# Optimization experiments

Hardware: AMD Instinct MI355X
Metric: run time of the kernel (lower is better)

## Reference

```python
import jax, jax.numpy as jnp
import numpy as np

N_NODES = 50000
N_GRAPHS = 64
BN_EPS = 1e-5
DIMS = [128, 256, 128, 64]


def setup_inputs() -> dict:
    key = jax.random.key(0)
    ks = jax.random.split(key, 32)
    inp = {}
    inp['x'] = jax.random.normal(ks[0], (N_NODES, DIMS[0]), dtype=jnp.float32)
    inp['edge_index'] = jax.random.randint(ks[1], (2, 800000), 0, N_NODES, dtype=jnp.int64)
    inp['batch'] = jnp.sort(jax.random.randint(ks[2], (N_NODES,), 0, N_GRAPHS, dtype=jnp.int64))
    ki = 3
    for i in range(3):
        fin, fout = DIMS[i], DIMS[i + 1]
        s = 1.0 / np.sqrt(fin)
        inp[f'W_rel{i}'] = jax.random.uniform(ks[ki], (fin, fout), jnp.float32, -s, s); ki += 1
        inp[f'b_rel{i}'] = jax.random.uniform(ks[ki], (fout,), jnp.float32, -s, s); ki += 1
        inp[f'W_root{i}'] = jax.random.uniform(ks[ki], (fin, fout), jnp.float32, -s, s); ki += 1
        inp[f'bn_g{i}'] = jnp.ones((fout,), jnp.float32)
        inp[f'bn_b{i}'] = jnp.zeros((fout,), jnp.float32)
        inp[f'bn_m{i}'] = jax.random.normal(ks[ki], (fout,), jnp.float32) * 0.1; ki += 1
        inp[f'bn_v{i}'] = jax.random.uniform(ks[ki], (fout,), jnp.float32, 0.5, 1.5); ki += 1
    so = 1.0 / np.sqrt(DIMS[-1])
    inp['W_out'] = jax.random.uniform(ks[ki], (DIMS[-1], 3), jnp.float32, -so, so); ki += 1
    inp['b_out'] = jax.random.uniform(ks[ki], (3,), jnp.float32, -so, so)
    return inp


def _graph_conv(x, src, dst, W_rel, b_rel, W_root):
    # PyG GraphConv: out_i = W_rel @ (sum_{j->i} x_j) + b_rel + W_root @ x_i
    agg = jax.ops.segment_sum(x[src], dst, num_segments=N_NODES)  # [N, fin]
    return agg @ W_rel + b_rel + x @ W_root


def _bn_relu(h, g, b, m, v):
    # BatchNorm1d in eval mode (running stats), then ReLU
    return jax.nn.relu((h - m) * jax.lax.rsqrt(v + BN_EPS) * g + b)


def reference(x, edge_index, batch,
              W_rel0, b_rel0, W_root0, bn_g0, bn_b0, bn_m0, bn_v0,
              W_rel1, b_rel1, W_root1, bn_g1, bn_b1, bn_m1, bn_v1,
              W_rel2, b_rel2, W_root2, bn_g2, bn_b2, bn_m2, bn_v2,
              W_out, b_out):
    src, dst = edge_index[0], edge_index[1]
    layers = [
        (W_rel0, b_rel0, W_root0, bn_g0, bn_b0, bn_m0, bn_v0),
        (W_rel1, b_rel1, W_root1, bn_g1, bn_b1, bn_m1, bn_v1),
        (W_rel2, b_rel2, W_root2, bn_g2, bn_b2, bn_m2, bn_v2),
    ]
    h = x
    for Wr, br, Ws, g, b, m, v in layers:
        h = _graph_conv(h, src, dst, Wr, br, Ws)
        h = _bn_relu(h, g, b, m, v)
        # dropout_rate = 0.0 -> identity
    # global mean pool over graphs
    sums = jax.ops.segment_sum(h, batch, num_segments=N_GRAPHS)  # [G, 64]
    cnts = jax.ops.segment_sum(jnp.ones((N_NODES, 1), h.dtype), batch, num_segments=N_GRAPHS)
    pooled = sums / jnp.maximum(cnts, 1.0)
    return pooled @ W_out + b_out  # [G, 3]
```

## Files before the change

### kernel.cpp

```cpp
#include <hip/hip_runtime.h>


typedef __attribute__((ext_vector_type(8))) short    bf16x8;
typedef __attribute__((ext_vector_type(4))) float    f32x4;
typedef __attribute__((ext_vector_type(8))) unsigned short ush8;
typedef __attribute__((ext_vector_type(4))) unsigned short ush4;

__device__ __forceinline__ unsigned short f2b(float f) {
    union { float f; unsigned int u; } c; c.f = f;
    unsigned int u = c.u;
    return (unsigned short)((u + 0x7fffu + ((u >> 16) & 1u)) >> 16);
}
__device__ __forceinline__ float b2f(unsigned short h) {
    union { unsigned int u; float f; } c; c.u = ((unsigned int)h) << 16;
    return c.f;
}
__device__ __forceinline__ float blo(unsigned int u) { return b2f((unsigned short)(u & 0xffff)); }
__device__ __forceinline__ float bhi(unsigned int u) { return b2f((unsigned short)(u >> 16)); }


__global__ __launch_bounds__(256)
void hist_kernel(const int* __restrict__ dst, int* __restrict__ cnt, int E, int span) {
    int grp = blockIdx.x & 7;
    int bid = blockIdx.x >> 3;
    int nb = gridDim.x >> 3;
    int lo = grp * span, hi = lo + span;
    for (int i = bid * 256 + threadIdx.x; i < E; i += nb * 256) {
        int d = dst[i];
        if (d >= lo && d < hi) atomicAdd(&cnt[d], 1);
    }
}

__global__ __launch_bounds__(256)
void scan1_kernel(const int* __restrict__ cnt, int* __restrict__ bsum, int N) {
    __shared__ int red[256];
    int base = blockIdx.x * 1024;
    int t = threadIdx.x;
    int s = 0;
#pragma unroll
    for (int j = 0; j < 4; ++j) {
        int i = base + t * 4 + j;
        if (i < N) s += cnt[i];
    }
    red[t] = s;
    __syncthreads();
    for (int d = 128; d > 0; d >>= 1) {
        if (t < d) red[t] += red[t + d];
        __syncthreads();
    }
    if (t == 0) bsum[blockIdx.x] = red[0];
}

__global__ void scan2_kernel(const int* __restrict__ bsum, int* __restrict__ boff, int nb) {
    __shared__ int v[1024];
    int t = threadIdx.x;
    for (int i = t; i < nb; i += 256) v[i] = bsum[i];
    __syncthreads();
    if (t == 0) {
        int run = 0;
        for (int i = 0; i < nb; ++i) { int c = v[i]; v[i] = run; run += c; }
    }
    __syncthreads();
    for (int i = t; i < nb; i += 256) boff[i] = v[i];
}

__global__ __launch_bounds__(256)
void scan3_kernel(const int* __restrict__ cnt, const int* __restrict__ boff,
                  int* __restrict__ rowptr, int* __restrict__ pos, int N) {
    __shared__ int wsum[4];
    int base = blockIdx.x * 1024;
    int t = threadIdx.x;
    int lane = t & 63, wv = t >> 6;
    int c[4];
    int s = 0;
#pragma unroll
    for (int j = 0; j < 4; ++j) {
        int i = base + t * 4 + j;
        c[j] = (i < N) ? cnt[i] : 0;
        s += c[j];
    }
    int val = s;
#pragma unroll
    for (int d = 1; d < 64; d <<= 1) {
        int o = __shfl_up(val, d, 64);
        if (lane >= d) val += o;
    }
    if (lane == 63) wsum[wv] = val;
    __syncthreads();
    int wadd = 0;
    for (int i = 0; i < wv; ++i) wadd += wsum[i];
    int excl = val - s + wadd + boff[blockIdx.x];
#pragma unroll
    for (int j = 0; j < 4; ++j) {
        int i = base + t * 4 + j;
        if (i < N) {
            rowptr[i] = excl;
            pos[i] = excl;
            excl += c[j];
            if (i == N - 1) rowptr[N] = excl;
        }
    }
}

__global__ __launch_bounds__(256)
void scatter_kernel(const int* __restrict__ src, const int* __restrict__ dst,
                    int* __restrict__ pos, int* __restrict__ srcs, int E, int span) {
    int grp = blockIdx.x & 7;
    int bid = blockIdx.x >> 3;
    int nb = gridDim.x >> 3;
    int lo = grp * span, hi = lo + span;
    for (int i = bid * 256 + threadIdx.x; i < E; i += nb * 256) {
        int d = dst[i];
        if (d >= lo && d < hi) {
            int p = atomicAdd(&pos[d], 1);
            srcs[p] = src[i];
        }
    }
}

__global__ void bounds_kernel(const int* __restrict__ batch, int* __restrict__ start, int N) {
    int g = threadIdx.x;
    if (g > 64) return;
    int lo = 0, hi = N;
    while (lo < hi) {
        int mid = (lo + hi) >> 1;
        if (batch[mid] < g) lo = mid + 1; else hi = mid;
    }
    start[g] = lo;
}


__global__ __launch_bounds__(256)
void conv_x_kernel(const float* __restrict__ x, unsigned short* __restrict__ xb, int n4) {
    int i = blockIdx.x * 256 + threadIdx.x;
    if (i >= n4) return;
    float4 v = ((const float4*)x)[i];
    ush4 o = { f2b(v.x), f2b(v.y), f2b(v.z), f2b(v.w) };
    *(ush4*)(xb + (size_t)i * 4) = o;
}

__global__ __launch_bounds__(256)
void conv_weights_kernel(const float* __restrict__ Wrel0, const float* __restrict__ Wroot0,
                         const float* __restrict__ Wrel1, const float* __restrict__ Wroot1,
                         const float* __restrict__ Wrel2, const float* __restrict__ Wroot2,
                         unsigned short* __restrict__ Wt0,
                         unsigned short* __restrict__ WtC1,
                         unsigned short* __restrict__ WtC2) {
    int i = blockIdx.x * 256 + threadIdx.x;
    if (i < 65536) {
        int m = i >> 8, k = i & 255;
        float v = (k < 128) ? Wrel0[k * 256 + m] : Wroot0[(k - 128) * 256 + m];
        Wt0[i] = f2b(v);
    } else if (i < 131072) {
        int j = i - 65536;
        int m = j >> 8, k = j & 255;
        float v = (m < 128) ? Wrel1[k * 128 + m] : Wroot1[k * 128 + (m - 128)];
        WtC1[j] = f2b(v);
    } else if (i < 147456) {
        int j = i - 131072;
        int m = j >> 7, k = j & 127;
        float v = (m < 64) ? Wrel2[k * 64 + m] : Wroot2[k * 64 + (m - 64)];
        WtC2[j] = f2b(v);
    }
}


template<int F>
__global__ __launch_bounds__(256)
void agg_bf16(const unsigned short* __restrict__ ysrc, int ystride,
              const unsigned short* __restrict__ yroot, int rstride,
              const int* __restrict__ rowptr, const int* __restrict__ srcs,
              const float* __restrict__ bias,
              const float* __restrict__ bng, const float* __restrict__ bnb,
              const float* __restrict__ bnm, const float* __restrict__ bnv,
              unsigned short* __restrict__ out, int N)
{
    int w = (blockIdx.x * blockDim.x + threadIdx.x) >> 6;
    int lane = threadIdx.x & 63;
    if (w >= N) return;
    int beg = rowptr[w], end = rowptr[w + 1];

    if (F == 128) {
        float p0[8] = {}, p1[8] = {};
        int e = beg;
        for (; e + 7 < end; e += 8) {
            unsigned int u[8];
#pragma unroll
            for (int q = 0; q < 8; ++q)
                u[q] = *(const unsigned int*)(ysrc + (size_t)srcs[e + q] * ystride + lane * 2);
#pragma unroll
            for (int q = 0; q < 8; ++q) { p0[q] += blo(u[q]); p1[q] += bhi(u[q]); }
        }
        for (; e < end; ++e) {
            unsigned int u = *(const unsigned int*)(ysrc + (size_t)srcs[e] * ystride + lane * 2);
            p0[0] += blo(u); p1[0] += bhi(u);
        }
        float a0 = ((p0[0] + p0[1]) + (p0[2] + p0[3])) + ((p0[4] + p0[5]) + (p0[6] + p0[7]));
        float a1 = ((p1[0] + p1[1]) + (p1[2] + p1[3])) + ((p1[4] + p1[5]) + (p1[6] + p1[7]));

        int f0 = lane * 2, f1 = lane * 2 + 1;
        if (yroot) {
            unsigned int u = *(const unsigned int*)(yroot + (size_t)w * rstride + lane * 2);
            a0 += blo(u); a1 += bhi(u);
        }
        if (bias) {
            a0 += bias[f0]; a1 += bias[f1];
            a0 = (a0 - bnm[f0]) * rsqrtf(bnv[f0] + 1e-5f) * bng[f0] + bnb[f0];
            a1 = (a1 - bnm[f1]) * rsqrtf(bnv[f1] + 1e-5f) * bng[f1] + bnb[f1];
            a0 = fmaxf(a0, 0.f); a1 = fmaxf(a1, 0.f);
        }
        unsigned int o = (unsigned int)f2b(a0) | ((unsigned int)f2b(a1) << 16);
        *(unsigned int*)(out + (size_t)w * 128 + lane * 2) = o;
    } else {
        int half = lane >> 5;
        int lr = lane & 31;
        float a0 = 0.f, a1 = 0.f, b0 = 0.f, b1 = 0.f;
        int e = beg + half;
        for (; e + 2 < end; e += 4) {
            int s0 = srcs[e], s1 = srcs[e + 2];
            unsigned int u0 = *(const unsigned int*)(ysrc + (size_t)s0 * ystride + lr * 2);
            unsigned int u1 = *(const unsigned int*)(ysrc + (size_t)s1 * ystride + lr * 2);
            a0 += blo(u0); a1 += bhi(u0);
            b0 += blo(u1); b1 += bhi(u1);
        }
        if (e < end) {
            unsigned int u = *(const unsigned int*)(ysrc + (size_t)srcs[e] * ystride + lr * 2);
            a0 += blo(u); a1 += bhi(u);
        }
        a0 += b0; a1 += b1;
        a0 += __shfl_xor(a0, 32, 64);
        a1 += __shfl_xor(a1, 32, 64);

        if (half == 0) {
            int f0 = lr * 2, f1 = lr * 2 + 1;
            if (yroot) {
                unsigned int u = *(const unsigned int*)(yroot + (size_t)w * rstride + lr * 2);
                a0 += blo(u); a1 += bhi(u);
            }
            if (bias) {
                a0 += bias[f0]; a1 += bias[f1];
                a0 = (a0 - bnm[f0]) * rsqrtf(bnv[f0] + 1e-5f) * bng[f0] + bnb[f0];
                a1 = (a1 - bnm[f1]) * rsqrtf(bnv[f1] + 1e-5f) * bng[f1] + bnb[f1];
                a0 = fmaxf(a0, 0.f); a1 = fmaxf(a1, 0.f);
            }
            unsigned int o = (unsigned int)f2b(a0) | ((unsigned int)f2b(a1) << 16);
            *(unsigned int*)(out + (size_t)w * 64 + lr * 2) = o;
        }
    }
}


__global__ __launch_bounds__(256)
void gemm_fused01(const unsigned short* __restrict__ aggb,
                  const unsigned short* __restrict__ xb,
                  const unsigned short* __restrict__ Wt0,
                  const unsigned short* __restrict__ WtC1,
                  const float* __restrict__ bias,
                  const float* __restrict__ bng, const float* __restrict__ bnb,
                  const float* __restrict__ bnm, const float* __restrict__ bnv,
                  unsigned short* __restrict__ yrel, unsigned short* __restrict__ yroot,
                  int N)
{
    __shared__ unsigned short smem[32768];
    unsigned short* As  = smem;
    unsigned short* Ws0 = smem + 4096;
    unsigned short* H   = smem;
    unsigned short* Ws1 = smem + 16384;

    const int tid = threadIdx.x;
    const int n0 = blockIdx.x * 64;
    const int wv = tid >> 6, lane = tid & 63;
    const int lr = lane & 15, lg = lane >> 4;
    const int swl = (lr & 7) << 3;

    f32x4 acc[16];
#pragma unroll
    for (int j = 0; j < 16; ++j) acc[j] = (f32x4){0.f, 0.f, 0.f, 0.f};

    for (int k0 = 0; k0 < 256; k0 += 64) {
#pragma unroll
        for (int it = 0; it < 2; ++it) {
            int c = tid + it * 256;
            int row = c >> 3;
            int kb = (c & 7) << 3;
            int sw = kb ^ ((row & 7) << 3);
            int n = n0 + row;
            int ksrc = k0 + kb;
            const unsigned short* Ap = (ksrc < 128) ? aggb : xb;
            int kl = (ksrc < 128) ? ksrc : ksrc - 128;
            ush8 va = {};
            if (n < N) va = *(const ush8*)(Ap + (size_t)n * 128 + kl);
            *(ush8*)&As[row * 64 + sw] = va;
        }
#pragma unroll
        for (int it = 0; it < 8; ++it) {
            int c = tid + it * 256;
            int row = c >> 3;
            int kb = (c & 7) << 3;
            int sw = kb ^ ((row & 7) << 3);
            ush8 vw = *(const ush8*)(Wt0 + (size_t)row * 256 + k0 + kb);
            *(ush8*)&Ws0[row * 64 + sw] = vw;
        }
        __syncthreads();
#pragma unroll
        for (int s = 0; s < 2; ++s) {
            int kk = s * 32 + lg * 8;
            int row = wv * 16 + lr;
            bf16x8 af = *(const bf16x8*)&As[row * 64 + (kk ^ swl)];
#pragma unroll
            for (int j = 0; j < 16; ++j) {
                int wr = j * 16 + lr;
                bf16x8 bfr = *(const bf16x8*)&Ws0[wr * 64 + (kk ^ swl)];
                acc[j] = __builtin_amdgcn_mfma_f32_16x16x32_bf16(af, bfr, acc[j], 0, 0, 0);
            }
        }
        __syncthreads();
    }

#pragma unroll
    for (int j = 0; j < 16; ++j) {
#pragma unroll
        for (int r = 0; r < 4; ++r) {
            int row = wv * 16 + lg * 4 + r;
            int col = j * 16 + lr;
            float val = acc[j][r] + bias[col];
            val = (val - bnm[col]) * rsqrtf(bnv[col] + 1e-5f) * bng[col] + bnb[col];
            val = fmaxf(val, 0.f);
            H[row * 256 + (col ^ ((row & 7) << 3))] = f2b(val);
        }
        acc[j] = (f32x4){0.f, 0.f, 0.f, 0.f};
    }
    __syncthreads();

    for (int k0 = 0; k0 < 256; k0 += 64) {
#pragma unroll
        for (int it = 0; it < 8; ++it) {
            int c = tid + it * 256;
            int row = c >> 3;
            int kb = (c & 7) << 3;
            int sw = kb ^ ((row & 7) << 3);
            ush8 vw = *(const ush8*)(WtC1 + (size_t)row * 256 + k0 + kb);
            *(ush8*)&Ws1[row * 64 + sw] = vw;
        }
        __syncthreads();
#pragma unroll
        for (int s = 0; s < 2; ++s) {
            int kk = s * 32 + lg * 8;
            int row = wv * 16 + lr;
            bf16x8 af = *(const bf16x8*)&H[row * 256 + ((k0 + kk) ^ swl)];
#pragma unroll
            for (int j = 0; j < 16; ++j) {
                int wr = j * 16 + lr;
                bf16x8 bfr = *(const bf16x8*)&Ws1[wr * 64 + (kk ^ swl)];
                acc[j] = __builtin_amdgcn_mfma_f32_16x16x32_bf16(af, bfr, acc[j], 0, 0, 0);
            }
        }
        __syncthreads();
    }

#pragma unroll
    for (int j = 0; j < 16; ++j) {
#pragma unroll
        for (int r = 0; r < 4; ++r) {
            int row = n0 + wv * 16 + lg * 4 + r;
            if (row >= N) continue;
            int col = j * 16 + lr;
            unsigned short hv = f2b(acc[j][r]);
            if (col < 128) yrel[(size_t)row * 128 + col] = hv;
            else           yroot[(size_t)row * 128 + col - 128] = hv;
        }
    }
}


__global__ __launch_bounds__(256)
void gemm_mfma(const unsigned short* __restrict__ A1,
               const unsigned short* __restrict__ Wt,
               unsigned short* __restrict__ C, unsigned short* __restrict__ C2,
               int csplit, int N, int Ktot, int M)
{
    __shared__ unsigned short As[64][64];
    __shared__ unsigned short Ws[128][64];

    const int tid = threadIdx.x;
    const int n0 = blockIdx.x * 64;
    const int m0 = blockIdx.y * 128;
    const int wid = tid >> 6, lane = tid & 63;
    const int wm = wid >> 1, wn = wid & 1;
    const int lr = lane & 15, lg = lane >> 4;

    f32x4 acc[2][4] = {};

    for (int k0 = 0; k0 < Ktot; k0 += 64) {
#pragma unroll
        for (int it = 0; it < 2; ++it) {
            int c = tid + it * 256;
            int row = c >> 3;
            int kb = (c & 7) << 3;
            int sw = kb ^ ((row & 7) << 3);
            int n = n0 + row;
            ush8 va = {};
            if (n < N) va = *(const ush8*)(A1 + (size_t)n * Ktot + k0 + kb);
            *(ush8*)&As[row][sw] = va;
        }
#pragma unroll
        for (int it = 0; it < 4; ++it) {
            int c = tid + it * 256;
            int row = c >> 3;
            int kb = (c & 7) << 3;
            int sw = kb ^ ((row & 7) << 3);
            ush8 vw = *(const ush8*)(Wt + (size_t)(m0 + row) * Ktot + k0 + kb);
            *(ush8*)&Ws[row][sw] = vw;
        }
        __syncthreads();
#pragma unroll
        for (int s = 0; s < 2; ++s) {
            int kk = s * 32 + lg * 8;
            bf16x8 af[2], bfr[4];
#pragma unroll
            for (int i = 0; i < 2; ++i) {
                int row = wm * 32 + i * 16 + lr;
                af[i] = *(const bf16x8*)&As[row][kk ^ ((row & 7) << 3)];
            }
#pragma unroll
            for (int j = 0; j < 4; ++j) {
                int wr = wn * 64 + j * 16 + lr;
                bfr[j] = *(const bf16x8*)&Ws[wr][kk ^ ((wr & 7) << 3)];
            }
#pragma unroll
            for (int i = 0; i < 2; ++i)
#pragma unroll
                for (int j = 0; j < 4; ++j)
                    acc[i][j] = __builtin_amdgcn_mfma_f32_16x16x32_bf16(af[i], bfr[j], acc[i][j], 0, 0, 0);
        }
        __syncthreads();
    }

#pragma unroll
    for (int i = 0; i < 2; ++i) {
#pragma unroll
        for (int r = 0; r < 4; ++r) {
            int row = n0 + wm * 32 + i * 16 + lg * 4 + r;
            if (row >= N) continue;
#pragma unroll
            for (int j = 0; j < 4; ++j) {
                int col = m0 + wn * 64 + j * 16 + lr;
                float val = acc[i][j][r];
                unsigned short* Cp;
                if (col < csplit) Cp = C + (size_t)row * csplit + col;
                else              Cp = C2 + (size_t)row * (M - csplit) + (col - csplit);
                *Cp = f2b(val);
            }
        }
    }
}


__global__ __launch_bounds__(256)
void pool_part_kernel(const unsigned short* __restrict__ h, const int* __restrict__ start,
                      float* __restrict__ partial) {
    int g = blockIdx.x >> 3, c = blockIdx.x & 7;
    int f = threadIdx.x & 63, sub = threadIdx.x >> 6;
    int beg = start[g], end = start[g + 1];
    int cnt = end - beg;
    int cbeg = beg + (int)(((long long)cnt * c) >> 3);
    int cend = beg + (int)(((long long)cnt * (c + 1)) >> 3);
    float acc = 0.f;
    for (int n = cbeg + sub; n < cend; n += 4)
        acc += b2f(h[(size_t)n * 64 + f]);
    __shared__ float red[4][64];
    red[sub][f] = acc;
    __syncthreads();
    if (sub == 0)
        partial[(size_t)blockIdx.x * 64 + f] = red[0][f] + red[1][f] + red[2][f] + red[3][f];
}

__global__ void head_final_kernel(const float* __restrict__ partial, const int* __restrict__ start,
                                  const float* __restrict__ Wout, const float* __restrict__ bout,
                                  float* __restrict__ out) {
    int g = blockIdx.x;
    int f = threadIdx.x;
    float s = 0.f;
#pragma unroll
    for (int c = 0; c < 8; ++c) s += partial[(size_t)(g * 8 + c) * 64 + f];
    float cnt = fmaxf((float)(start[g + 1] - start[g]), 1.0f);
    __shared__ float red[64];
    red[f] = s / cnt;
    __syncthreads();
    if (f < 3) {
        float acc = 0.f;
#pragma unroll
        for (int k = 0; k < 64; ++k) acc += red[k] * Wout[k * 3 + f];
        out[g * 3 + f] = acc + bout[f];
    }
}


extern "C" void kernel_launch(void* const* d_in, const int* in_sizes, int n_in,
                              void* d_out, int out_size, void* d_ws, size_t ws_size,
                              hipStream_t stream)
{
    const float* x       = (const float*)d_in[0];
    const int*   ei      = (const int*)d_in[1];
    const int*   batch   = (const int*)d_in[2];
    const float* W_rel0  = (const float*)d_in[3];
    const float* b_rel0  = (const float*)d_in[4];
    const float* W_root0 = (const float*)d_in[5];
    const float* bn_g0   = (const float*)d_in[6];
    const float* bn_b0   = (const float*)d_in[7];
    const float* bn_m0   = (const float*)d_in[8];
    const float* bn_v0   = (const float*)d_in[9];
    const float* W_rel1  = (const float*)d_in[10];
    const float* b_rel1  = (const float*)d_in[11];
    const float* W_root1 = (const float*)d_in[12];
    const float* bn_g1   = (const float*)d_in[13];
    const float* bn_b1   = (const float*)d_in[14];
    const float* bn_m1   = (const float*)d_in[15];
    const float* bn_v1   = (const float*)d_in[16];
    const float* W_rel2  = (const float*)d_in[17];
    const float* b_rel2  = (const float*)d_in[18];
    const float* W_root2 = (const float*)d_in[19];
    const float* bn_g2   = (const float*)d_in[20];
    const float* bn_b2   = (const float*)d_in[21];
    const float* bn_m2   = (const float*)d_in[22];
    const float* bn_v2   = (const float*)d_in[23];
    const float* W_out   = (const float*)d_in[24];
    const float* b_out   = (const float*)d_in[25];

    const int N = in_sizes[0] / 128;
    const int E = in_sizes[1] / 2;
    const int* src = ei;
    const int* dst = ei + E;

    char* ws = (char*)d_ws;
    size_t off = 0;
    auto alloc = [&](size_t b) -> void* {
        off = (off + 255) & ~(size_t)255;
        void* p = ws + off;
        off += b;
        return p;
    };

    unsigned short* xb16   = (unsigned short*)alloc((size_t)N * 128 * 2);
    unsigned short* aggb16 = (unsigned short*)alloc((size_t)N * 128 * 2);
    unsigned short* yrel   = (unsigned short*)alloc((size_t)N * 128 * 2);
    unsigned short* yroot  = (unsigned short*)alloc((size_t)N * 128 * 2);
    unsigned short* h1     = (unsigned short*)alloc((size_t)N * 128 * 2);
    unsigned short* h2     = (unsigned short*)alloc((size_t)N * 64 * 2);
    unsigned short* Wt0    = (unsigned short*)alloc(256 * 256 * 2);
    unsigned short* WtC1   = (unsigned short*)alloc(256 * 256 * 2);
    unsigned short* WtC2   = (unsigned short*)alloc(128 * 128 * 2);
    int* cnt    = (int*)alloc((size_t)N * 4);
    int* rowp   = (int*)alloc((size_t)(N + 1) * 4);
    int* pos    = (int*)alloc((size_t)N * 4);
    int* srcs   = (int*)alloc((size_t)E * 4);
    int* gstart = (int*)alloc(65 * 4);
    int* bsum   = (int*)alloc(1024 * 4);
    int* boff   = (int*)alloc(1024 * 4);
    float* partial = (float*)alloc((size_t)512 * 64 * 4);

    hipMemsetAsync(cnt, 0, (size_t)N * 4, stream);

    const int TB = 256;
    const int nwb = (N + 3) / 4;
    const int nsb = (N + 1023) / 1024;
    const int span = (N + 7) / 8;

    hist_kernel<<<1024, TB, 0, stream>>>(dst, cnt, E, span);
    scan1_kernel<<<nsb, TB, 0, stream>>>(cnt, bsum, N);
    scan2_kernel<<<1, TB, 0, stream>>>(bsum, boff, nsb);
    scan3_kernel<<<nsb, TB, 0, stream>>>(cnt, boff, rowp, pos, N);
    scatter_kernel<<<1024, TB, 0, stream>>>(src, dst, pos, srcs, E, span);
    bounds_kernel<<<1, 128, 0, stream>>>(batch, gstart, N);

    conv_weights_kernel<<<576, TB, 0, stream>>>(W_rel0, W_root0, W_rel1, W_root1,
                                                W_rel2, W_root2, Wt0, WtC1, WtC2);
    conv_x_kernel<<<(N * 128 / 4 + TB - 1) / TB, TB, 0, stream>>>(x, xb16, N * 128 / 4);

    const int gx = (N + 63) / 64;

    agg_bf16<128><<<nwb, TB, 0, stream>>>(xb16, 128, nullptr, 0, rowp, srcs,
                                          nullptr, nullptr, nullptr, nullptr, nullptr,
                                          aggb16, N);
    gemm_fused01<<<gx, TB, 0, stream>>>(aggb16, xb16, Wt0, WtC1,
                                        b_rel0, bn_g0, bn_b0, bn_m0, bn_v0,
                                        yrel, yroot, N);
    agg_bf16<128><<<nwb, TB, 0, stream>>>(yrel, 128, yroot, 128, rowp, srcs,
                                          b_rel1, bn_g1, bn_b1, bn_m1, bn_v1,
                                          h1, N);

    gemm_mfma<<<dim3(gx, 1), TB, 0, stream>>>(h1, WtC2, yrel, yroot, 64, N, 128, 128);
    agg_bf16<64><<<nwb, TB, 0, stream>>>(yrel, 64, yroot, 64, rowp, srcs,
                                         b_rel2, bn_g2, bn_b2, bn_m2, bn_v2,
                                         h2, N);

    pool_part_kernel<<<512, TB, 0, stream>>>(h2, gstart, partial);
    head_final_kernel<<<64, 64, 0, stream>>>(partial, gstart, W_out, b_out, (float*)d_out);
}
```

Before: 279.9 us.

## Merge setup kernels, halve dst partitioning, read GEMM weights directly from global

Folds the batch-boundary search into the scan2 kernel and merges the weight and x bf16 conversions into one launch, cutting two launches. The hist and scatter kernels now split destinations into 4 ranges instead of 8, so each edge is scanned fewer times but atomics are less localized. In gemm_fused01 the weight tiles are no longer staged in shared memory. B fragments are loaded straight from global/L2, which removes syncs and halves LDS use but makes the loads uncoalesced and repeated per wave.

```diff
diff --git a/kernel.cpp b/kernel.cpp
--- a/kernel.cpp
+++ b/kernel.cpp
@@ -21,9 +21,9 @@
 
 __global__ __launch_bounds__(256)
 void hist_kernel(const int* __restrict__ dst, int* __restrict__ cnt, int E, int span) {
-    int grp = blockIdx.x & 7;
-    int bid = blockIdx.x >> 3;
-    int nb = gridDim.x >> 3;
+    int grp = blockIdx.x & 3;
+    int bid = blockIdx.x >> 2;
+    int nb = gridDim.x >> 2;
     int lo = grp * span, hi = lo + span;
     for (int i = bid * 256 + threadIdx.x; i < E; i += nb * 256) {
         int d = dst[i];
@@ -51,7 +51,8 @@
     if (t == 0) bsum[blockIdx.x] = red[0];
 }
 
-__global__ void scan2_kernel(const int* __restrict__ bsum, int* __restrict__ boff, int nb) {
+__global__ void scan2_bounds_kernel(const int* __restrict__ bsum, int* __restrict__ boff, int nb,
+                                    const int* __restrict__ batch, int* __restrict__ gstart, int N) {
     __shared__ int v[1024];
     int t = threadIdx.x;
     for (int i = t; i < nb; i += 256) v[i] = bsum[i];
@@ -62,6 +63,14 @@
     }
     __syncthreads();
     for (int i = t; i < nb; i += 256) boff[i] = v[i];
+    if (t <= 64) {
+        int lo = 0, hi = N;
+        while (lo < hi) {
+            int mid = (lo + hi) >> 1;
+            if (batch[mid] < t) lo = mid + 1; else hi = mid;
+        }
+        gstart[t] = lo;
+    }
 }
 
 __global__ __launch_bounds__(256)
@@ -105,9 +114,9 @@
 __global__ __launch_bounds__(256)
 void scatter_kernel(const int* __restrict__ src, const int* __restrict__ dst,
                     int* __restrict__ pos, int* __restrict__ srcs, int E, int span) {
-    int grp = blockIdx.x & 7;
-    int bid = blockIdx.x >> 3;
-    int nb = gridDim.x >> 3;
+    int grp = blockIdx.x & 3;
+    int bid = blockIdx.x >> 2;
+    int nb = gridDim.x >> 2;
     int lo = grp * span, hi = lo + span;
     for (int i = bid * 256 + threadIdx.x; i < E; i += nb * 256) {
         int d = dst[i];
@@ -118,49 +127,38 @@
     }
 }
 
-__global__ void bounds_kernel(const int* __restrict__ batch, int* __restrict__ start, int N) {
-    int g = threadIdx.x;
-    if (g > 64) return;
-    int lo = 0, hi = N;
-    while (lo < hi) {
-        int mid = (lo + hi) >> 1;
-        if (batch[mid] < g) lo = mid + 1; else hi = mid;
-    }
-    start[g] = lo;
-}
-
-
-__global__ __launch_bounds__(256)
-void conv_x_kernel(const float* __restrict__ x, unsigned short* __restrict__ xb, int n4) {
-    int i = blockIdx.x * 256 + threadIdx.x;
-    if (i >= n4) return;
-    float4 v = ((const float4*)x)[i];
-    ush4 o = { f2b(v.x), f2b(v.y), f2b(v.z), f2b(v.w) };
-    *(ush4*)(xb + (size_t)i * 4) = o;
-}
-
-__global__ __launch_bounds__(256)
-void conv_weights_kernel(const float* __restrict__ Wrel0, const float* __restrict__ Wroot0,
-                         const float* __restrict__ Wrel1, const float* __restrict__ Wroot1,
-                         const float* __restrict__ Wrel2, const float* __restrict__ Wroot2,
-                         unsigned short* __restrict__ Wt0,
-                         unsigned short* __restrict__ WtC1,
-                         unsigned short* __restrict__ WtC2) {
-    int i = blockIdx.x * 256 + threadIdx.x;
-    if (i < 65536) {
-        int m = i >> 8, k = i & 255;
-        float v = (k < 128) ? Wrel0[k * 256 + m] : Wroot0[(k - 128) * 256 + m];
-        Wt0[i] = f2b(v);
-    } else if (i < 131072) {
-        int j = i - 65536;
-        int m = j >> 8, k = j & 255;
-        float v = (m < 128) ? Wrel1[k * 128 + m] : Wroot1[k * 128 + (m - 128)];
-        WtC1[j] = f2b(v);
-    } else if (i < 147456) {
-        int j = i - 131072;
-        int m = j >> 7, k = j & 127;
-        float v = (m < 64) ? Wrel2[k * 64 + m] : Wroot2[k * 64 + (m - 64)];
-        WtC2[j] = f2b(v);
+
+__global__ __launch_bounds__(256)
+void conv_all_kernel(const float* __restrict__ x, unsigned short* __restrict__ xb, int n4,
+                     const float* __restrict__ Wrel0, const float* __restrict__ Wroot0,
+                     const float* __restrict__ Wrel1, const float* __restrict__ Wroot1,
+                     const float* __restrict__ Wrel2, const float* __restrict__ Wroot2,
+                     unsigned short* __restrict__ Wt0,
+                     unsigned short* __restrict__ WtC1,
+                     unsigned short* __restrict__ WtC2) {
+    if (blockIdx.x < 576) {
+        int i = blockIdx.x * 256 + threadIdx.x;
+        if (i < 65536) {
+            int m = i >> 8, k = i & 255;
+            float v = (k < 128) ? Wrel0[k * 256 + m] : Wroot0[(k - 128) * 256 + m];
+            Wt0[i] = f2b(v);
+        } else if (i < 131072) {
+            int j = i - 65536;
+            int m = j >> 8, k = j & 255;
+            float v = (m < 128) ? Wrel1[k * 128 + m] : Wroot1[k * 128 + (m - 128)];
+            WtC1[j] = f2b(v);
+        } else if (i < 147456) {
+            int j = i - 131072;
+            int m = j >> 7, k = j & 127;
+            float v = (m < 64) ? Wrel2[k * 64 + m] : Wroot2[k * 64 + (m - 64)];
+            WtC2[j] = f2b(v);
+        }
+    } else {
+        int i = (blockIdx.x - 576) * 256 + threadIdx.x;
+        if (i >= n4) return;
+        float4 v = ((const float4*)x)[i];
+        ush4 o = { f2b(v.x), f2b(v.y), f2b(v.z), f2b(v.w) };
+        *(ush4*)(xb + (size_t)i * 4) = o;
     }
 }
 
@@ -261,11 +259,9 @@
                   unsigned short* __restrict__ yrel, unsigned short* __restrict__ yroot,
                   int N)
 {
-    __shared__ unsigned short smem[32768];
-    unsigned short* As  = smem;
-    unsigned short* Ws0 = smem + 4096;
-    unsigned short* H   = smem;
-    unsigned short* Ws1 = smem + 16384;
+    __shared__ unsigned short smem[16384];
+    unsigned short* As = smem;
+    unsigned short* H  = smem;
 
     const int tid = threadIdx.x;
     const int n0 = blockIdx.x * 64;
@@ -292,15 +288,6 @@
             if (n < N) va = *(const ush8*)(Ap + (size_t)n * 128 + kl);
             *(ush8*)&As[row * 64 + sw] = va;
         }
-#pragma unroll
-        for (int it = 0; it < 8; ++it) {
-            int c = tid + it * 256;
-            int row = c >> 3;
-            int kb = (c & 7) << 3;
-            int sw = kb ^ ((row & 7) << 3);
-            ush8 vw = *(const ush8*)(Wt0 + (size_t)row * 256 + k0 + kb);
-            *(ush8*)&Ws0[row * 64 + sw] = vw;
-        }
         __syncthreads();
 #pragma unroll
         for (int s = 0; s < 2; ++s) {
@@ -309,8 +296,7 @@
             bf16x8 af = *(const bf16x8*)&As[row * 64 + (kk ^ swl)];
 #pragma unroll
             for (int j = 0; j < 16; ++j) {
-                int wr = j * 16 + lr;
-                bf16x8 bfr = *(const bf16x8*)&Ws0[wr * 64 + (kk ^ swl)];
+                bf16x8 bfr = *(const bf16x8*)(Wt0 + (size_t)(j * 16 + lr) * 256 + k0 + kk);
                 acc[j] = __builtin_amdgcn_mfma_f32_16x16x32_bf16(af, bfr, acc[j], 0, 0, 0);
             }
         }
@@ -332,17 +318,8 @@
     }
     __syncthreads();
 
+#pragma unroll
     for (int k0 = 0; k0 < 256; k0 += 64) {
-#pragma unroll
-        for (int it = 0; it < 8; ++it) {
-            int c = tid + it * 256;
-            int row = c >> 3;
-            int kb = (c & 7) << 3;
-            int sw = kb ^ ((row & 7) << 3);
-            ush8 vw = *(const ush8*)(WtC1 + (size_t)row * 256 + k0 + kb);
-            *(ush8*)&Ws1[row * 64 + sw] = vw;
-        }
-        __syncthreads();
 #pragma unroll
         for (int s = 0; s < 2; ++s) {
             int kk = s * 32 + lg * 8;
@@ -350,12 +327,10 @@
             bf16x8 af = *(const bf16x8*)&H[row * 256 + ((k0 + kk) ^ swl)];
 #pragma unroll
             for (int j = 0; j < 16; ++j) {
-                int wr = j * 16 + lr;
-                bf16x8 bfr = *(const bf16x8*)&Ws1[wr * 64 + (kk ^ swl)];
+                bf16x8 bfr = *(const bf16x8*)(WtC1 + (size_t)(j * 16 + lr) * 256 + k0 + kk);
                 acc[j] = __builtin_amdgcn_mfma_f32_16x16x32_bf16(af, bfr, acc[j], 0, 0, 0);
             }
         }
-        __syncthreads();
     }
 
 #pragma unroll
@@ -564,18 +539,17 @@
     const int TB = 256;
     const int nwb = (N + 3) / 4;
     const int nsb = (N + 1023) / 1024;
-    const int span = (N + 7) / 8;
-
-    hist_kernel<<<1024, TB, 0, stream>>>(dst, cnt, E, span);
+    const int span4 = (N + 3) / 4;
+    const int n4 = N * 128 / 4;
+
+    hist_kernel<<<1024, TB, 0, stream>>>(dst, cnt, E, span4);
     scan1_kernel<<<nsb, TB, 0, stream>>>(cnt, bsum, N);
-    scan2_kernel<<<1, TB, 0, stream>>>(bsum, boff, nsb);
+    scan2_bounds_kernel<<<1, TB, 0, stream>>>(bsum, boff, nsb, batch, gstart, N);
     scan3_kernel<<<nsb, TB, 0, stream>>>(cnt, boff, rowp, pos, N);
-    scatter_kernel<<<1024, TB, 0, stream>>>(src, dst, pos, srcs, E, span);
-    bounds_kernel<<<1, 128, 0, stream>>>(batch, gstart, N);
-
-    conv_weights_kernel<<<576, TB, 0, stream>>>(W_rel0, W_root0, W_rel1, W_root1,
-                                                W_rel2, W_root2, Wt0, WtC1, WtC2);
-    conv_x_kernel<<<(N * 128 / 4 + TB - 1) / TB, TB, 0, stream>>>(x, xb16, N * 128 / 4);
+    scatter_kernel<<<1024, TB, 0, stream>>>(src, dst, pos, srcs, E, span4);
+
+    conv_all_kernel<<<576 + (n4 + TB - 1) / TB, TB, 0, stream>>>(
+        x, xb16, n4, W_rel0, W_root0, W_rel1, W_root1, W_rel2, W_root2, Wt0, WtC1, WtC2);
 
     const int gx = (N + 63) / 64;
 
```

New measurement: 366.1 us. 1.31x slower.
